# Kernel tuning notes

Hardware: AMD Instinct MI355X
Metric: run time of the kernel (lower is better)

## Reference

```python
import jax, jax.numpy as jnp
import numpy as np

BLOCK = 128
FP8_MAX = 448.0  # max representable value of float8_e4m3fn
F8 = jnp.float8_e4m3fn


def setup_inputs() -> dict:
    key = jax.random.key(0)
    k1, k2, k3 = jax.random.split(key, 3)
    M, K, N = 4096, 7168, 16384
    x = jax.random.normal(k1, (M, K), jnp.float32)
    w = jax.random.normal(k2, (N, K), jnp.float32)  # raw weight; cast to fp8 in reference to simulate stored fp8
    w_scale = jax.random.uniform(k3, (N // BLOCK, K // BLOCK), jnp.float32, 0.5, 1.5)
    return {"x": x, "w": w, "w_scale": w_scale, "block_size": BLOCK}


def act_quant(x, b):
    M, K = x.shape
    xb = x.reshape(M, K // b, b)
    s = jnp.max(jnp.abs(xb), axis=-1) / FP8_MAX  # [M, K//b]
    xq = (xb / s[..., None]).astype(F8).astype(jnp.float32).reshape(M, K)
    return xq, s


def reference(x, w, w_scale, block_size):
    b = block_size
    # simulate fp8-stored weight (element_size == 1 branch)
    w8 = w.astype(F8).astype(jnp.float32)  # [N, K]
    # fp8_gemm: y[m,n] = sum_k xq[m,k]*w8[n,k]*xs[m,kb]*ws[nb,kb]
    # scales factor per-element, so dequantize both operands then one dense GEMM
    xq, xs = act_quant(x, b)
    x_dq = xq * jnp.repeat(xs, b, axis=1)                         # [M, K]
    w_dq = w8 * jnp.repeat(jnp.repeat(w_scale, b, axis=0), b, axis=1)  # [N, K]
    return x_dq @ w_dq.T  # [M, N], no bias (bias=False)
```

## Files before the change

### kernel.cpp

```cpp
#include <hip/hip_runtime.h>
#include <hip/hip_bf16.h>
#include <hip/hip_fp8.h>

typedef __attribute__((ext_vector_type(8))) short short8;
typedef __attribute__((ext_vector_type(4))) float f32x4;

#define AS1 __attribute__((address_space(1)))
#define AS3 __attribute__((address_space(3)))

static constexpr int Mdim = 4096;
static constexpr int Kdim = 7168;
static constexpr int Ndim = 16384;
static constexpr float FP8_MAX = 448.0f;

#define BARRIER() do { asm volatile("" ::: "memory"); \
                       __builtin_amdgcn_s_barrier();  \
                       asm volatile("" ::: "memory"); } while (0)

#define MFMA_BF16 __builtin_amdgcn_mfma_f32_16x16x32_bf16

__global__ __launch_bounds__(256) void quant_x_kernel(
    const float* __restrict__ x, __hip_bfloat16* __restrict__ xdq)
{
    constexpr int NBLK = Mdim * (Kdim / 128);
    const int lane = threadIdx.x & 63;
    const int wid  = (blockIdx.x * 256 + threadIdx.x) >> 6;
    const int nw   = (gridDim.x * 256) >> 6;

    for (int b = wid; b < NBLK; b += nw) {
        size_t base = (size_t)b * 128 + lane * 2;
        float2 v = *reinterpret_cast<const float2*>(x + base);
        float amax = fmaxf(fabsf(v.x), fabsf(v.y));
#pragma unroll
        for (int off = 32; off > 0; off >>= 1)
            amax = fmaxf(amax, __shfl_xor(amax, off));
        float s = amax * (1.0f / FP8_MAX);
        float q0 = 0.0f, q1 = 0.0f;
        if (s > 0.0f) {
            q0 = (float)__hip_fp8_e4m3(v.x / s) * s;
            q1 = (float)__hip_fp8_e4m3(v.y / s) * s;
        }
        __hip_bfloat162 o;
        o.x = __float2bfloat16(q0);
        o.y = __float2bfloat16(q1);
        *reinterpret_cast<__hip_bfloat162*>(xdq + base) = o;
    }
}

__global__ __launch_bounds__(256) void quant_w_kernel(
    const float* __restrict__ w, const float* __restrict__ ws,
    __hip_bfloat16* __restrict__ wdq)
{
    constexpr size_t NCHUNK = (size_t)Ndim * Kdim / 8;
    constexpr int CPR = Kdim / 8;
    constexpr int KB  = Kdim / 128;

    size_t idx    = (size_t)blockIdx.x * 256 + threadIdx.x;
    size_t stride = (size_t)gridDim.x * 256;

    for (size_t c = idx; c < NCHUNK; c += stride) {
        int n  = (int)(c / CPR);
        int kc = (int)(c - (size_t)n * CPR);
        int k  = kc * 8;
        float s = ws[(n >> 7) * KB + (k >> 7)];
        const float* src = w + (size_t)n * Kdim + k;
        float4 v0 = *reinterpret_cast<const float4*>(src);
        float4 v1 = *reinterpret_cast<const float4*>(src + 4);

        __hip_bfloat16 h[8];
        h[0] = __float2bfloat16((float)__hip_fp8_e4m3(v0.x) * s);
        h[1] = __float2bfloat16((float)__hip_fp8_e4m3(v0.y) * s);
        h[2] = __float2bfloat16((float)__hip_fp8_e4m3(v0.z) * s);
        h[3] = __float2bfloat16((float)__hip_fp8_e4m3(v0.w) * s);
        h[4] = __float2bfloat16((float)__hip_fp8_e4m3(v1.x) * s);
        h[5] = __float2bfloat16((float)__hip_fp8_e4m3(v1.y) * s);
        h[6] = __float2bfloat16((float)__hip_fp8_e4m3(v1.z) * s);
        h[7] = __float2bfloat16((float)__hip_fp8_e4m3(v1.w) * s);
        *reinterpret_cast<short8*>(wdq + (size_t)n * Kdim + k) =
            *reinterpret_cast<short8*>(h);
    }
}

constexpr int BM = 256, BN = 256, BK = 64;
constexpr int NT  = Kdim / BK;
constexpr int NBN = Ndim / BN;
constexpr int NWG = (Mdim / BM) * NBN;
constexpr int K2  = Kdim * 2;

__global__ __launch_bounds__(512, 2) void gemm256_kernel(
    const __hip_bfloat16* __restrict__ Ag,
    const __hip_bfloat16* __restrict__ Bg,
    float* __restrict__ C)
{
    extern __shared__ char smem[];

    const int tid  = threadIdx.x;
    const int w    = tid >> 6;
    const int lane = tid & 63;
    const int wr   = w >> 2;
    const int wc   = w & 3;
    const int lr   = lane & 15;
    const int lk   = lane >> 4;

    int bid = (int)blockIdx.x;
    int swz = (bid & 7) * (NWG >> 3) + (bid >> 3);
    const int bm = (swz / NBN) * BM;
    const int bn = (swz % NBN) * BN;

    const int sw   = (lr & 7) << 4;
    const int col0 = (lk * 16) ^ sw;
    const int col1 = (64 + lk * 16) ^ sw;
    const int bRow = (wc & 1) * 64;

    size_t offG[2];
    int    ldsW[2];
#pragma unroll
    for (int q = 0; q < 2; ++q) {
        int chp  = (w * 2 + q) * 64 + lane;
        int row  = chp >> 3;
        int colb = ((chp & 7) ^ (row & 7)) * 16;
        offG[q]  = (size_t)row * K2 + colb;
        ldsW[q]  = (w * 2 + q) * 1024;
    }
    const char* Ab = (const char*)Ag + (size_t)bm * K2;
    const char* Bb = (const char*)Bg + (size_t)bn * K2;

    auto stage = [&](int j) {
        if (j >= 4 * NT) return;
        const int T    = j >> 2;
        const int r    = j & 3;
        const int isA  = r >> 1;
        const int half = r & 1;
        const int regByte = (T & 1) * 65536 + (isA ? 0 : 32768) + half * 16384;
        const char* g = (isA ? Ab : Bb) + (size_t)half * (128 * (size_t)K2)
                        + (size_t)T * 128;
#pragma unroll
        for (int q = 0; q < 2; ++q)
            __builtin_amdgcn_global_load_lds((const AS1 void*)(g + offG[q]),
                                             (AS3 void*)(smem + regByte + ldsW[q]),
                                             16, 0, 0);
    };

    for (int j = 0; j < 6; ++j) stage(j);
    asm volatile("s_waitcnt vmcnt(4)" ::: "memory");
    BARRIER();

    f32x4 acc[8][4] = {};

    for (int t = 0; t < NT; ++t) {
        const int buf = t & 1;
        const char* aB = smem + buf * 65536 + wr * 16384;
        const char* bB = smem + buf * 65536 + 32768 + (wc >> 1) * 16384;
        short8 a0[4][2], a1[4][2], b0[2][2], b1[2][2];

        stage(4 * t + 6);
#pragma unroll
        for (int m = 0; m < 4; ++m) {
            const char* p = aB + (m * 16 + lr) * 128;
            a0[m][0] = *(const short8*)(p + col0);
            a0[m][1] = *(const short8*)(p + col1);
        }
#pragma unroll
        for (int n = 0; n < 2; ++n) {
            const char* p = bB + (bRow + n * 16 + lr) * 128;
            b0[n][0] = *(const short8*)(p + col0);
            b0[n][1] = *(const short8*)(p + col1);
        }
        __builtin_amdgcn_s_setprio(1);
#pragma unroll
        for (int m = 0; m < 4; ++m)
#pragma unroll
            for (int n = 0; n < 2; ++n) {
                acc[m][n] = MFMA_BF16(a0[m][0], b0[n][0], acc[m][n], 0, 0, 0);
                acc[m][n] = MFMA_BF16(a0[m][1], b0[n][1], acc[m][n], 0, 0, 0);
            }
        __builtin_amdgcn_s_setprio(0);

        stage(4 * t + 7);
#pragma unroll
        for (int n = 0; n < 2; ++n) {
            const char* p = bB + (bRow + (n + 2) * 16 + lr) * 128;
            b1[n][0] = *(const short8*)(p + col0);
            b1[n][1] = *(const short8*)(p + col1);
        }
        __builtin_amdgcn_s_setprio(1);
#pragma unroll
        for (int m = 0; m < 4; ++m)
#pragma unroll
            for (int n = 0; n < 2; ++n) {
                acc[m][n + 2] = MFMA_BF16(a0[m][0], b1[n][0], acc[m][n + 2], 0, 0, 0);
                acc[m][n + 2] = MFMA_BF16(a0[m][1], b1[n][1], acc[m][n + 2], 0, 0, 0);
            }
        __builtin_amdgcn_s_setprio(0);
        BARRIER();

        stage(4 * t + 8);
#pragma unroll
        for (int m = 0; m < 4; ++m) {
            const char* p = aB + ((m + 4) * 16 + lr) * 128;
            a1[m][0] = *(const short8*)(p + col0);
            a1[m][1] = *(const short8*)(p + col1);
        }
        __builtin_amdgcn_s_setprio(1);
#pragma unroll
        for (int m = 0; m < 4; ++m)
#pragma unroll
            for (int n = 0; n < 2; ++n) {
                acc[m + 4][n] = MFMA_BF16(a1[m][0], b0[n][0], acc[m + 4][n], 0, 0, 0);
                acc[m + 4][n] = MFMA_BF16(a1[m][1], b0[n][1], acc[m + 4][n], 0, 0, 0);
            }
        __builtin_amdgcn_s_setprio(0);

        stage(4 * t + 9);
        __builtin_amdgcn_s_setprio(1);
#pragma unroll
        for (int m = 0; m < 4; ++m)
#pragma unroll
            for (int n = 0; n < 2; ++n) {
                acc[m + 4][n + 2] = MFMA_BF16(a1[m][0], b1[n][0], acc[m + 4][n + 2], 0, 0, 0);
                acc[m + 4][n + 2] = MFMA_BF16(a1[m][1], b1[n][1], acc[m + 4][n + 2], 0, 0, 0);
            }
        __builtin_amdgcn_s_setprio(0);
        if (t < NT - 2) { asm volatile("s_waitcnt vmcnt(4)" ::: "memory"); }
        else            { asm volatile("s_waitcnt vmcnt(0)" ::: "memory"); }
        BARRIER();
    }

#pragma unroll
    for (int m = 0; m < 8; ++m) {
#pragma unroll
        for (int n = 0; n < 4; ++n) {
            const int row0 = bm + wr * 128 + m * 16 + lk * 4;
            const int col  = bn + wc * 64 + n * 16 + lr;
#pragma unroll
            for (int j = 0; j < 4; ++j)
                C[(size_t)(row0 + j) * Ndim + col] = acc[m][n][j];
        }
    }
}

extern "C" void kernel_launch(void* const* d_in, const int* in_sizes, int n_in,
                              void* d_out, int out_size, void* d_ws, size_t ws_size,
                              hipStream_t stream) {
    const float* x  = (const float*)d_in[0];
    const float* w  = (const float*)d_in[1];
    const float* ws = (const float*)d_in[2];

    __hip_bfloat16* xdq = (__hip_bfloat16*)d_ws;
    __hip_bfloat16* wdq = xdq + (size_t)Mdim * Kdim;

    quant_x_kernel<<<2048, 256, 0, stream>>>(x, xdq);
    quant_w_kernel<<<4096, 256, 0, stream>>>(w, ws, wdq);

    hipFuncSetAttribute((const void*)gemm256_kernel,
                        hipFuncAttributeMaxDynamicSharedMemorySize, 131072);
    gemm256_kernel<<<NWG, 512, 131072, stream>>>(xdq, wdq, (float*)d_out);
}
```

Measured before the change: 956.2 us.

## Switch GEMM to native FP8 MFMA with per-block scale application in accumulator

The quantization kernels now emit raw fp8 bytes plus a transposed per-row activation scale array, instead of dequantized bf16. The GEMM uses the fp8 16x16x32 MFMA on 1-byte operands and halves LDS and global traffic. Each K-block's partial product goes into a temporary accumulator that is multiplied by the activation and weight scales, then added to the running sum. The cost is extra vector FMA work per MFMA pair and scale loads inside the main loop.

```diff
diff --git a/kernel.cpp b/kernel.cpp
--- a/kernel.cpp
+++ b/kernel.cpp
@@ -2,7 +2,6 @@
 #include <hip/hip_bf16.h>
 #include <hip/hip_fp8.h>
 
-typedef __attribute__((ext_vector_type(8))) short short8;
 typedef __attribute__((ext_vector_type(4))) float f32x4;
 
 #define AS1 __attribute__((address_space(1)))
@@ -11,18 +10,20 @@
 static constexpr int Mdim = 4096;
 static constexpr int Kdim = 7168;
 static constexpr int Ndim = 16384;
+static constexpr int KB   = Kdim / 128;
 static constexpr float FP8_MAX = 448.0f;
 
 #define BARRIER() do { asm volatile("" ::: "memory"); \
                        __builtin_amdgcn_s_barrier();  \
                        asm volatile("" ::: "memory"); } while (0)
 
-#define MFMA_BF16 __builtin_amdgcn_mfma_f32_16x16x32_bf16
+#define MFMA_FP8 __builtin_amdgcn_mfma_f32_16x16x32_fp8_fp8
 
 __global__ __launch_bounds__(256) void quant_x_kernel(
-    const float* __restrict__ x, __hip_bfloat16* __restrict__ xdq)
+    const float* __restrict__ x, unsigned char* __restrict__ xq,
+    float* __restrict__ xst)
 {
-    constexpr int NBLK = Mdim * (Kdim / 128);
+    constexpr int NBLK = Mdim * KB;
     const int lane = threadIdx.x & 63;
     const int wid  = (blockIdx.x * 256 + threadIdx.x) >> 6;
     const int nw   = (gridDim.x * 256) >> 6;
@@ -35,49 +36,42 @@
         for (int off = 32; off > 0; off >>= 1)
             amax = fmaxf(amax, __shfl_xor(amax, off));
         float s = amax * (1.0f / FP8_MAX);
-        float q0 = 0.0f, q1 = 0.0f;
+        unsigned char q0 = 0, q1 = 0;
         if (s > 0.0f) {
-            q0 = (float)__hip_fp8_e4m3(v.x / s) * s;
-            q1 = (float)__hip_fp8_e4m3(v.y / s) * s;
-        }
-        __hip_bfloat162 o;
-        o.x = __float2bfloat16(q0);
-        o.y = __float2bfloat16(q1);
-        *reinterpret_cast<__hip_bfloat162*>(xdq + base) = o;
+            q0 = __hip_fp8_e4m3(v.x / s).__x;
+            q1 = __hip_fp8_e4m3(v.y / s).__x;
+        }
+        *reinterpret_cast<unsigned short*>(xq + base) =
+            (unsigned short)(q0 | ((unsigned short)q1 << 8));
+        if (lane == 0) {
+            int row = b / KB, kb = b - row * KB;
+            xst[(size_t)kb * Mdim + row] = s;
+        }
     }
 }
 
 __global__ __launch_bounds__(256) void quant_w_kernel(
-    const float* __restrict__ w, const float* __restrict__ ws,
-    __hip_bfloat16* __restrict__ wdq)
+    const float* __restrict__ w, unsigned char* __restrict__ w8)
 {
     constexpr size_t NCHUNK = (size_t)Ndim * Kdim / 8;
-    constexpr int CPR = Kdim / 8;
-    constexpr int KB  = Kdim / 128;
 
     size_t idx    = (size_t)blockIdx.x * 256 + threadIdx.x;
     size_t stride = (size_t)gridDim.x * 256;
 
     for (size_t c = idx; c < NCHUNK; c += stride) {
-        int n  = (int)(c / CPR);
-        int kc = (int)(c - (size_t)n * CPR);
-        int k  = kc * 8;
-        float s = ws[(n >> 7) * KB + (k >> 7)];
-        const float* src = w + (size_t)n * Kdim + k;
+        const float* src = w + c * 8;
         float4 v0 = *reinterpret_cast<const float4*>(src);
         float4 v1 = *reinterpret_cast<const float4*>(src + 4);
-
-        __hip_bfloat16 h[8];
-        h[0] = __float2bfloat16((float)__hip_fp8_e4m3(v0.x) * s);
-        h[1] = __float2bfloat16((float)__hip_fp8_e4m3(v0.y) * s);
-        h[2] = __float2bfloat16((float)__hip_fp8_e4m3(v0.z) * s);
-        h[3] = __float2bfloat16((float)__hip_fp8_e4m3(v0.w) * s);
-        h[4] = __float2bfloat16((float)__hip_fp8_e4m3(v1.x) * s);
-        h[5] = __float2bfloat16((float)__hip_fp8_e4m3(v1.y) * s);
-        h[6] = __float2bfloat16((float)__hip_fp8_e4m3(v1.z) * s);
-        h[7] = __float2bfloat16((float)__hip_fp8_e4m3(v1.w) * s);
-        *reinterpret_cast<short8*>(wdq + (size_t)n * Kdim + k) =
-            *reinterpret_cast<short8*>(h);
+        unsigned int lo = (unsigned int)__hip_fp8_e4m3(v0.x).__x
+                        | ((unsigned int)__hip_fp8_e4m3(v0.y).__x << 8)
+                        | ((unsigned int)__hip_fp8_e4m3(v0.z).__x << 16)
+                        | ((unsigned int)__hip_fp8_e4m3(v0.w).__x << 24);
+        unsigned int hi = (unsigned int)__hip_fp8_e4m3(v1.x).__x
+                        | ((unsigned int)__hip_fp8_e4m3(v1.y).__x << 8)
+                        | ((unsigned int)__hip_fp8_e4m3(v1.z).__x << 16)
+                        | ((unsigned int)__hip_fp8_e4m3(v1.w).__x << 24);
+        uint2 p; p.x = lo; p.y = hi;
+        *reinterpret_cast<uint2*>(w8 + c * 8) = p;
     }
 }
 
@@ -85,11 +79,13 @@
 constexpr int NT  = Kdim / BK;
 constexpr int NBN = Ndim / BN;
 constexpr int NWG = (Mdim / BM) * NBN;
-constexpr int K2  = Kdim * 2;
-
-__global__ __launch_bounds__(512, 2) void gemm256_kernel(
-    const __hip_bfloat16* __restrict__ Ag,
-    const __hip_bfloat16* __restrict__ Bg,
+constexpr int K1  = Kdim;
+
+__global__ __launch_bounds__(512, 2) void gemm256_fp8_kernel(
+    const unsigned char* __restrict__ Ag,
+    const unsigned char* __restrict__ Bg,
+    const float* __restrict__ xsT,
+    const float* __restrict__ Wsc,
     float* __restrict__ C)
 {
     extern __shared__ char smem[];
@@ -107,23 +103,21 @@
     const int bm = (swz / NBN) * BM;
     const int bn = (swz % NBN) * BN;
 
-    const int sw   = (lr & 7) << 4;
-    const int col0 = (lk * 16) ^ sw;
-    const int col1 = (64 + lk * 16) ^ sw;
+    const int sw   = ((lr >> 1) & 3) << 4;
+    const int col0 = (lk * 8) ^ sw;
+    const int col1 = (32 + lk * 8) ^ sw;
     const int bRow = (wc & 1) * 64;
 
-    size_t offG[2];
-    int    ldsW[2];
-#pragma unroll
-    for (int q = 0; q < 2; ++q) {
-        int chp  = (w * 2 + q) * 64 + lane;
-        int row  = chp >> 3;
-        int colb = ((chp & 7) ^ (row & 7)) * 16;
-        offG[q]  = (size_t)row * K2 + colb;
-        ldsW[q]  = (w * 2 + q) * 1024;
-    }
-    const char* Ab = (const char*)Ag + (size_t)bm * K2;
-    const char* Bb = (const char*)Bg + (size_t)bn * K2;
+    const int nb  = (bn + wc * 64) >> 7;
+    const int rsb = bm + wr * 128 + lk * 4;
+
+    const int rowS = tid >> 2;
+    const int colS = (((tid & 3) ^ ((rowS >> 1) & 3))) * 16;
+    const size_t offG = (size_t)rowS * K1 + colS;
+    const int ldsW = tid * 16;
+
+    const char* Ab = (const char*)Ag + (size_t)bm * K1;
+    const char* Bb = (const char*)Bg + (size_t)bn * K1;
 
     auto stage = [&](int j) {
         if (j >= 4 * NT) return;
@@ -131,65 +125,77 @@
         const int r    = j & 3;
         const int isA  = r >> 1;
         const int half = r & 1;
-        const int regByte = (T & 1) * 65536 + (isA ? 0 : 32768) + half * 16384;
-        const char* g = (isA ? Ab : Bb) + (size_t)half * (128 * (size_t)K2)
-                        + (size_t)T * 128;
-#pragma unroll
-        for (int q = 0; q < 2; ++q)
-            __builtin_amdgcn_global_load_lds((const AS1 void*)(g + offG[q]),
-                                             (AS3 void*)(smem + regByte + ldsW[q]),
-                                             16, 0, 0);
+        const int regByte = (T & 1) * 32768 + (isA ? 0 : 16384) + half * 8192;
+        const char* g = (isA ? Ab : Bb) + (size_t)half * (128 * (size_t)K1)
+                        + (size_t)T * 64 + offG;
+        __builtin_amdgcn_global_load_lds((const AS1 void*)g,
+                                         (AS3 void*)(smem + regByte + ldsW),
+                                         16, 0, 0);
     };
 
     for (int j = 0; j < 6; ++j) stage(j);
-    asm volatile("s_waitcnt vmcnt(4)" ::: "memory");
+    asm volatile("s_waitcnt vmcnt(2)" ::: "memory");
     BARRIER();
 
     f32x4 acc[8][4] = {};
 
     for (int t = 0; t < NT; ++t) {
         const int buf = t & 1;
-        const char* aB = smem + buf * 65536 + wr * 16384;
-        const char* bB = smem + buf * 65536 + 32768 + (wc >> 1) * 16384;
-        short8 a0[4][2], a1[4][2], b0[2][2], b1[2][2];
+        const int kb  = t >> 1;
+        const char* aB = smem + buf * 32768 + wr * 8192;
+        const char* bB = smem + buf * 32768 + 16384 + (wc >> 1) * 8192;
+        long long a0[4][2], a1[4][2], b0[2][2], b1[2][2];
+        f32x4 sv[4];
+
+        const float wsv = Wsc[nb * KB + kb];
+        const float* xrow = xsT + (size_t)kb * Mdim + rsb;
 
         stage(4 * t + 6);
 #pragma unroll
         for (int m = 0; m < 4; ++m) {
-            const char* p = aB + (m * 16 + lr) * 128;
-            a0[m][0] = *(const short8*)(p + col0);
-            a0[m][1] = *(const short8*)(p + col1);
+            const char* p = aB + (m * 16 + lr) * 64;
+            a0[m][0] = *(const long long*)(p + col0);
+            a0[m][1] = *(const long long*)(p + col1);
         }
 #pragma unroll
         for (int n = 0; n < 2; ++n) {
-            const char* p = bB + (bRow + n * 16 + lr) * 128;
-            b0[n][0] = *(const short8*)(p + col0);
-            b0[n][1] = *(const short8*)(p + col1);
-        }
-        __builtin_amdgcn_s_setprio(1);
-#pragma unroll
-        for (int m = 0; m < 4; ++m)
-#pragma unroll
-            for (int n = 0; n < 2; ++n) {
-                acc[m][n] = MFMA_BF16(a0[m][0], b0[n][0], acc[m][n], 0, 0, 0);
-                acc[m][n] = MFMA_BF16(a0[m][1], b0[n][1], acc[m][n], 0, 0, 0);
+            const char* p = bB + (bRow + n * 16 + lr) * 64;
+            b0[n][0] = *(const long long*)(p + col0);
+            b0[n][1] = *(const long long*)(p + col1);
+        }
+#pragma unroll
+        for (int m = 0; m < 4; ++m) {
+            f32x4 s = *reinterpret_cast<const f32x4*>(xrow + m * 16);
+            sv[m] = s * wsv;
+        }
+        __builtin_amdgcn_s_setprio(1);
+#pragma unroll
+        for (int m = 0; m < 4; ++m)
+#pragma unroll
+            for (int n = 0; n < 2; ++n) {
+                f32x4 pacc = {0.f, 0.f, 0.f, 0.f};
+                pacc = MFMA_FP8(a0[m][0], b0[n][0], pacc, 0, 0, 0);
+                pacc = MFMA_FP8(a0[m][1], b0[n][1], pacc, 0, 0, 0);
+                acc[m][n] += sv[m] * pacc;
             }
         __builtin_amdgcn_s_setprio(0);
 
         stage(4 * t + 7);
 #pragma unroll
         for (int n = 0; n < 2; ++n) {
-            const char* p = bB + (bRow + (n + 2) * 16 + lr) * 128;
-            b1[n][0] = *(const short8*)(p + col0);
-            b1[n][1] = *(const short8*)(p + col1);
-        }
-        __builtin_amdgcn_s_setprio(1);
-#pragma unroll
-        for (int m = 0; m < 4; ++m)
-#pragma unroll
-            for (int n = 0; n < 2; ++n) {
-                acc[m][n + 2] = MFMA_BF16(a0[m][0], b1[n][0], acc[m][n + 2], 0, 0, 0);
-                acc[m][n + 2] = MFMA_BF16(a0[m][1], b1[n][1], acc[m][n + 2], 0, 0, 0);
+            const char* p = bB + (bRow + (n + 2) * 16 + lr) * 64;
+            b1[n][0] = *(const long long*)(p + col0);
+            b1[n][1] = *(const long long*)(p + col1);
+        }
+        __builtin_amdgcn_s_setprio(1);
+#pragma unroll
+        for (int m = 0; m < 4; ++m)
+#pragma unroll
+            for (int n = 0; n < 2; ++n) {
+                f32x4 pacc = {0.f, 0.f, 0.f, 0.f};
+                pacc = MFMA_FP8(a0[m][0], b1[n][0], pacc, 0, 0, 0);
+                pacc = MFMA_FP8(a0[m][1], b1[n][1], pacc, 0, 0, 0);
+                acc[m][n + 2] += sv[m] * pacc;
             }
         __builtin_amdgcn_s_setprio(0);
         BARRIER();
@@ -197,17 +203,24 @@
         stage(4 * t + 8);
 #pragma unroll
         for (int m = 0; m < 4; ++m) {
-            const char* p = aB + ((m + 4) * 16 + lr) * 128;
-            a1[m][0] = *(const short8*)(p + col0);
-            a1[m][1] = *(const short8*)(p + col1);
-        }
-        __builtin_amdgcn_s_setprio(1);
-#pragma unroll
-        for (int m = 0; m < 4; ++m)
-#pragma unroll
-            for (int n = 0; n < 2; ++n) {
-                acc[m + 4][n] = MFMA_BF16(a1[m][0], b0[n][0], acc[m + 4][n], 0, 0, 0);
-                acc[m + 4][n] = MFMA_BF16(a1[m][1], b0[n][1], acc[m + 4][n], 0, 0, 0);
+            const char* p = aB + ((m + 4) * 16 + lr) * 64;
+            a1[m][0] = *(const long long*)(p + col0);
+            a1[m][1] = *(const long long*)(p + col1);
+        }
+#pragma unroll
+        for (int m = 0; m < 4; ++m) {
+            f32x4 s = *reinterpret_cast<const f32x4*>(xrow + 64 + m * 16);
+            sv[m] = s * wsv;
+        }
+        __builtin_amdgcn_s_setprio(1);
+#pragma unroll
+        for (int m = 0; m < 4; ++m)
+#pragma unroll
+            for (int n = 0; n < 2; ++n) {
+                f32x4 pacc = {0.f, 0.f, 0.f, 0.f};
+                pacc = MFMA_FP8(a1[m][0], b0[n][0], pacc, 0, 0, 0);
+                pacc = MFMA_FP8(a1[m][1], b0[n][1], pacc, 0, 0, 0);
+                acc[m + 4][n] += sv[m] * pacc;
             }
         __builtin_amdgcn_s_setprio(0);
 
@@ -217,11 +230,13 @@
         for (int m = 0; m < 4; ++m)
 #pragma unroll
             for (int n = 0; n < 2; ++n) {
-                acc[m + 4][n + 2] = MFMA_BF16(a1[m][0], b1[n][0], acc[m + 4][n + 2], 0, 0, 0);
-                acc[m + 4][n + 2] = MFMA_BF16(a1[m][1], b1[n][1], acc[m + 4][n + 2], 0, 0, 0);
-            }
-        __builtin_amdgcn_s_setprio(0);
-        if (t < NT - 2) { asm volatile("s_waitcnt vmcnt(4)" ::: "memory"); }
+                f32x4 pacc = {0.f, 0.f, 0.f, 0.f};
+                pacc = MFMA_FP8(a1[m][0], b1[n][0], pacc, 0, 0, 0);
+                pacc = MFMA_FP8(a1[m][1], b1[n][1], pacc, 0, 0, 0);
+                acc[m + 4][n + 2] += sv[m] * pacc;
+            }
+        __builtin_amdgcn_s_setprio(0);
+        if (t < NT - 2) { asm volatile("s_waitcnt vmcnt(2)" ::: "memory"); }
         else            { asm volatile("s_waitcnt vmcnt(0)" ::: "memory"); }
         BARRIER();
     }
@@ -246,13 +261,15 @@
     const float* w  = (const float*)d_in[1];
     const float* ws = (const float*)d_in[2];
 
-    __hip_bfloat16* xdq = (__hip_bfloat16*)d_ws;
-    __hip_bfloat16* wdq = xdq + (size_t)Mdim * Kdim;
-
-    quant_x_kernel<<<2048, 256, 0, stream>>>(x, xdq);
-    quant_w_kernel<<<4096, 256, 0, stream>>>(w, ws, wdq);
-
-    hipFuncSetAttribute((const void*)gemm256_kernel,
-                        hipFuncAttributeMaxDynamicSharedMemorySize, 131072);
-    gemm256_kernel<<<NWG, 512, 131072, stream>>>(xdq, wdq, (float*)d_out);
-}
+    unsigned char* xq  = (unsigned char*)d_ws;
+    unsigned char* w8  = xq + (size_t)Mdim * Kdim;
+    float*         xst = (float*)(w8 + (size_t)Ndim * Kdim);
+
+    quant_x_kernel<<<2048, 256, 0, stream>>>(x, xq, xst);
+    quant_w_kernel<<<4096, 256, 0, stream>>>(w, w8);
+
+    hipFuncSetAttribute((const void*)gemm256_fp8_kernel,
+                        hipFuncAttributeMaxDynamicSharedMemorySize, 65536);
+    gemm256_fp8_kernel<<<NWG, 512, 65536, stream>>>(xq, w8, xst, ws,
+                                                    (float*)d_out);
+}
```

New measurement: 1.391 ms. +45.5%, slower.
